# Optimization experiments

Hardware: AMD Instinct MI355X
Metric: run time of the kernel (lower is better)

## Reference

```python
import jax, jax.numpy as jnp
import numpy as np

H = 4  # heads


def _tconv(x, src, dst, ea, Wq, bq, Wk, bk, Wv, bv, We, Ws, bs):
    # PyG TransformerConv, heads=4, concat=False, root_weight=True, beta=False
    N = x.shape[0]
    Dh = Wq.shape[1] // H  # per-head dim (= hidden_channels)
    q = (x @ Wq + bq).reshape(N, H, Dh)
    k = (x @ Wk + bk).reshape(N, H, Dh)
    v = (x @ Wv + bv).reshape(N, H, Dh)
    e = (ea @ We).reshape(-1, H, Dh)      # lin_edge has no bias in PyG
    kj = k[src] + e                        # [E, H, Dh]
    vj = v[src] + e                        # [E, H, Dh]
    alpha = (q[dst] * kj).sum(-1) / jnp.sqrt(jnp.asarray(Dh, x.dtype))  # [E, H]
    # segment softmax over incoming edges of each dst node
    m = jax.ops.segment_max(alpha, dst, num_segments=N)
    a = jnp.exp(alpha - m[dst])
    s = jax.ops.segment_sum(a, dst, num_segments=N)
    a = a / (s[dst] + 1e-16)
    out = jax.ops.segment_sum(a[:, :, None] * vj, dst, num_segments=N)  # [N, H, Dh]
    out = out.mean(axis=1)                 # concat=False -> mean over heads
    return out + x @ Ws + bs               # root/skip connection


def setup_inputs() -> dict:
    key = jax.random.key(0)
    ks = jax.random.split(key, 32)
    N, E, C_in, C_e, Ch = 50000, 800000, 32, 16, 32
    d = {}
    d['x'] = jax.random.normal(ks[0], (N, C_in), dtype=jnp.float32)
    d['edge_attr'] = jax.random.normal(ks[1], (E, C_e), dtype=jnp.float32)
    d['edge_index'] = jax.random.randint(ks[2], (2, E), 0, N, dtype=jnp.int32)
    s = 0.05
    i = 3
    for L, cin in ((1, C_in), (2, Ch)):
        d[f'Wq{L}'] = jax.random.normal(ks[i], (cin, H * Ch)) * s; i += 1
        d[f'bq{L}'] = jnp.zeros((H * Ch,), jnp.float32)
        d[f'Wk{L}'] = jax.random.normal(ks[i], (cin, H * Ch)) * s; i += 1
        d[f'bk{L}'] = jnp.zeros((H * Ch,), jnp.float32)
        d[f'Wv{L}'] = jax.random.normal(ks[i], (cin, H * Ch)) * s; i += 1
        d[f'bv{L}'] = jnp.zeros((H * Ch,), jnp.float32)
        d[f'We{L}'] = jax.random.normal(ks[i], (C_e, H * Ch)) * s; i += 1
        d[f'Ws{L}'] = jax.random.normal(ks[i], (cin, Ch)) * s; i += 1
        d[f'bs{L}'] = jnp.zeros((Ch,), jnp.float32)
    d['Wm1'] = jax.random.normal(ks[i], (2 * Ch + C_e, Ch)) * s; i += 1
    d['bm1'] = jnp.zeros((Ch,), jnp.float32)
    d['Wm2'] = jax.random.normal(ks[i], (Ch, 1)) * s; i += 1
    d['bm2'] = jnp.zeros((1,), jnp.float32)
    return d


def reference(x, edge_attr, edge_index,
              Wq1, bq1, Wk1, bk1, Wv1, bv1, We1, Ws1, bs1,
              Wq2, bq2, Wk2, bk2, Wv2, bv2, We2, Ws2, bs2,
              Wm1, bm1, Wm2, bm2):
    src, dst = edge_index[0], edge_index[1]
    h = jax.nn.relu(_tconv(x, src, dst, edge_attr, Wq1, bq1, Wk1, bk1, Wv1, bv1, We1, Ws1, bs1))
    h = jax.nn.relu(_tconv(h, src, dst, edge_attr, Wq2, bq2, Wk2, bk2, Wv2, bv2, We2, Ws2, bs2))
    ef = jnp.concatenate([h[src], edge_attr, h[dst]], axis=-1)  # [E, 2*Ch + C_e]
    out = jax.nn.relu(ef @ Wm1 + bm1) @ Wm2 + bm2
    return out.reshape(-1)
```

## Files before the change

### kernel.cpp

```cpp
#include <hip/hip_runtime.h>
#include <hip/hip_fp16.h>
#include <math.h>

#define D128 128
#define CH32 32
#define CE16 16

__global__ void k_hist(const int* __restrict__ dst, int* __restrict__ deg, int E) {
    int e = blockIdx.x * blockDim.x + threadIdx.x;
    if (e < E) atomicAdd(&deg[dst[e]], 1);
}

__global__ void k_scan1(const int* __restrict__ deg, int* __restrict__ offs,
                        int* __restrict__ bsum, int N) {
    __shared__ int buf[256];
    int t = threadIdx.x;
    int i = blockIdx.x * 256 + t;
    int v = (i < N) ? deg[i] : 0;
    buf[t] = v;
    __syncthreads();
    #pragma unroll
    for (int off = 1; off < 256; off <<= 1) {
        int val = (t >= off) ? buf[t - off] : 0;
        __syncthreads();
        buf[t] += val;
        __syncthreads();
    }
    if (i < N) offs[i] = buf[t] - v;
    if (t == 255) bsum[blockIdx.x] = buf[255];
}

__global__ void k_scan2(const int* __restrict__ bsum, int* __restrict__ boff, int nb) {
    __shared__ int buf[256];
    int t = threadIdx.x;
    int v = (t < nb) ? bsum[t] : 0;
    buf[t] = v;
    __syncthreads();
    #pragma unroll
    for (int off = 1; off < 256; off <<= 1) {
        int val = (t >= off) ? buf[t - off] : 0;
        __syncthreads();
        buf[t] += val;
        __syncthreads();
    }
    if (t < nb) boff[t] = buf[t] - v;
}

__global__ void k_scan3(const int* __restrict__ boff, int* __restrict__ offs,
                        int* __restrict__ cur, int N, int E) {
    int i = blockIdx.x * blockDim.x + threadIdx.x;
    if (i < N) {
        int o = offs[i] + boff[i >> 8];
        offs[i] = o;
        cur[i] = o;
    }
    if (i == 0) offs[N] = E;
}

__global__ void k_scatter_idx(const int* __restrict__ src, const int* __restrict__ dst,
                              int* __restrict__ cur, int* __restrict__ csr_srcb,
                              int2* __restrict__ csr_de, int E) {
    int e = blockIdx.x * blockDim.x + threadIdx.x;
    if (e < E) {
        int d = dst[e];
        int p = atomicAdd(&cur[d], 1);
        csr_srcb[p] = src[e] << 9;
        csr_de[p] = make_int2(d, e);
    }
}

__global__ __launch_bounds__(256) void k_gather_ea(
    const float4* __restrict__ ea4, const int2* __restrict__ csr_de,
    float4* __restrict__ ea_csr4, int E) {
    int idx = blockIdx.x * 256 + threadIdx.x;
    int p = idx >> 2, q = idx & 3;
    if (p < E) {
        int e = csr_de[p].y;
        ea_csr4[idx] = ea4[e * 4 + q];
    }
}

__global__ void k_wqe(const float* __restrict__ Wq1, const float* __restrict__ bq1,
                      const float* __restrict__ We1,
                      const float* __restrict__ Wq2, const float* __restrict__ bq2,
                      const float* __restrict__ We2,
                      float* __restrict__ Wqe1, float* __restrict__ bqe1,
                      float* __restrict__ Wqe2, float* __restrict__ bqe2) {
    int t = threadIdx.x, h = t >> 4, j = t & 15;
    const float QS = 0.17677669529663687f * 1.4426950408889634f;
    int b = blockIdx.x;
    int layer = (b >= 33);
    int i = layer ? b - 33 : b;
    const float* Wq = layer ? Wq2 : Wq1;
    const float* bq = layer ? bq2 : bq1;
    const float* We = layer ? We2 : We1;
    float* Wqe = layer ? Wqe2 : Wqe1;
    float* bqe = layer ? bqe2 : bqe1;
    const float* base = (i < 32) ? (Wq + i * D128) : bq;
    float s = 0.f;
    #pragma unroll
    for (int d = 0; d < 32; d++)
        s = fmaf(base[h * 32 + d], We[j * D128 + h * 32 + d], s);
    s *= QS;
    if (i < 32) Wqe[i * 64 + t] = s;
    else        bqe[t] = s;
}

__global__ __launch_bounds__(128) void k_nodeproj(
    const float* __restrict__ xin,
    const float* __restrict__ Wq, const float* __restrict__ bq,
    const float* __restrict__ Wk, const float* __restrict__ bk,
    const float* __restrict__ Wv, const float* __restrict__ bv,
    const float* __restrict__ Ws, const float* __restrict__ bs,
    const float* __restrict__ Wqe, const float* __restrict__ bqe,
    float* __restrict__ q, __half* __restrict__ kvh,
    float* __restrict__ skip, float* __restrict__ qeb, int N)
{
    int tid = threadIdx.x;
    int c   = tid & 31;
    int pos = ((tid >> 2) << 3) | (tid & 3);
    float wq[32], wk[32], wv[32], ws[32];
    #pragma unroll
    for (int j = 0; j < 32; j++) {
        wq[j] = Wq[j * D128 + tid];
        wk[j] = Wk[j * D128 + tid];
        wv[j] = Wv[j * D128 + tid];
        ws[j] = Ws[j * CH32 + c];
    }
    float bqc = bq[tid], bkc = bk[tid], bvc = bv[tid], bsc = bs[c];
    __shared__ float wqeS[32][64];
    __shared__ float xs[4][32];
    for (int i = tid; i < 2048; i += 128) wqeS[i >> 6][i & 63] = Wqe[i];
    float bqec = bqe[tid & 63];
    int nchunk = (N + 3) / 4;
    for (int chk = blockIdx.x; chk < nchunk; chk += gridDim.x) {
        int base = chk * 4;
        {
            int r = tid >> 5;
            int n = base + r;
            xs[r][c] = (n < N) ? xin[n * 32 + c] : 0.f;
        }
        __syncthreads();
        #pragma unroll
        for (int r = 0; r < 4; r++) {
            int n = base + r;
            if (n < N) {
                float aq = bqc, ak = bkc, av = bvc;
                #pragma unroll
                for (int j = 0; j < 32; j++) {
                    float xj = xs[r][j];
                    aq = fmaf(xj, wq[j], aq);
                    ak = fmaf(xj, wk[j], ak);
                    av = fmaf(xj, wv[j], av);
                }
                q[n * D128 + tid] = aq;
                kvh[(size_t)n * 256 + pos]     = __float2half_rn(ak);
                kvh[(size_t)n * 256 + pos + 4] = __float2half_rn(av);
            }
        }
        {
            int r = tid >> 5;
            int n = base + r;
            if (n < N) {
                float as = bsc;
                #pragma unroll
                for (int j = 0; j < 32; j++) as = fmaf(xs[r][j], ws[j], as);
                skip[n * 32 + c] = as;
            }
        }
        {
            int c6 = tid & 63;
            int r0 = (tid >> 6) << 1;
            #pragma unroll
            for (int rr = 0; rr < 2; rr++) {
                int n = base + r0 + rr;
                if (n < N) {
                    float a = bqec;
                    #pragma unroll
                    for (int j = 0; j < 32; j++)
                        a = fmaf(xs[r0 + rr][j], wqeS[j][c6], a);
                    qeb[(size_t)n * 64 + c6] = a;
                }
            }
        }
        __syncthreads();
    }
}

__global__ __launch_bounds__(64) void k_edgeattn(
    const float* __restrict__ q, const __half* __restrict__ kvh,
    const float* __restrict__ skip,
    const float* __restrict__ ea_csr, const float* __restrict__ We,
    const int* __restrict__ offs, const int* __restrict__ csr_srcb,
    const float* __restrict__ qeb, float* __restrict__ hout)
{
    int node = blockIdx.x;
    int lane = threadIdx.x;
    int eg   = lane >> 5;
    int c    = lane & 31;
    int g    = c & 7;
    int c4   = c << 2;

    const float QS = 0.17677669529663687f * 1.4426950408889634f;
    float4 qv = *(const float4*)&q[(size_t)node * D128 + c4];
    qv.x *= QS; qv.y *= QS; qv.z *= QS; qv.w *= QS;

    float2 qe01 = *(const float2*)&qeb[(size_t)node * 64 + ((c >> 3) << 4) + 2 * g];
    float qe0 = qe01.x, qe1 = qe01.y;

    int s0 = offs[node], s1 = offs[node + 1];
    int deg = s1 - s0;

    float l = 0.f;
    float ac0 = 0.f, ac1 = 0.f, ac2 = 0.f, ac3 = 0.f;
    float se0 = 0.f, se1 = 0.f;

    if (deg > 0) {
        int last = s1 - 1;
        const char* kvb = (const char*)kvh;
        int toff = c << 4;

        auto eidx = [&](int p) { return min(s0 + 2 * p + eg, last); };
        auto ldidx = [&](int p) { return csr_srcb[eidx(p)]; };
        auto ldkv  = [&](int ib) {
            return *(const float4*)(kvb + (size_t)(unsigned)ib + toff);
        };
        auto ldea  = [&](int p) {
            return *(const float2*)&ea_csr[(size_t)eidx(p) * 16 + 2 * g];
        };
        auto pair = [&](const float4& kvr, const float2& eav, int p) {
            bool valid = (s0 + 2 * p + eg) <= last;
            float2 k01 = __half22float2(*(const __half2*)&kvr.x);
            float2 k23 = __half22float2(*(const __half2*)&kvr.y);
            float2 v01 = __half22float2(*(const __half2*)&kvr.z);
            float2 v23 = __half22float2(*(const __half2*)&kvr.w);
            float t = fmaf(qv.y, k01.y, qv.x * k01.x);
            t = fmaf(qv.z, k23.x, t);
            t = fmaf(qv.w, k23.y, t);
            t = fmaf(qe0, eav.x, t);
            t = fmaf(qe1, eav.y, t);
            t += __shfl_xor(t, 1);
            t += __shfl_xor(t, 2);
            t += __shfl_xor(t, 4);
            float pp = valid ? __builtin_amdgcn_exp2f(t) : 0.f;
            l += pp;
            ac0 = fmaf(pp, v01.x, ac0);
            ac1 = fmaf(pp, v01.y, ac1);
            ac2 = fmaf(pp, v23.x, ac2);
            ac3 = fmaf(pp, v23.y, ac3);
            se0 = fmaf(pp, eav.x, se0);
            se1 = fmaf(pp, eav.y, se1);
        };

        int iA0 = ldidx(0), iA1 = ldidx(1);
        int iB0 = ldidx(2), iB1 = ldidx(3);
        float4 kA0 = ldkv(iA0), kA1 = ldkv(iA1);
        float2 eA0 = ldea(0),   eA1 = ldea(1);

        int p = 0;
        int nIter = (deg + 7) >> 3;
        for (int it = 0; it < nIter; ++it) {
            float4 kB0 = ldkv(iB0), kB1 = ldkv(iB1);
            float2 eB0 = ldea(p + 2), eB1 = ldea(p + 3);
            iA0 = ldidx(p + 4); iA1 = ldidx(p + 5);

            pair(kA0, eA0, p + 0);
            pair(kA1, eA1, p + 1);

            kA0 = ldkv(iA0); kA1 = ldkv(iA1);
            eA0 = ldea(p + 4); eA1 = ldea(p + 5);
            iB0 = ldidx(p + 6); iB1 = ldidx(p + 7);

            pair(kB0, eB0, p + 2);
            pair(kB1, eB1, p + 3);

            p += 4;
        }
    }

    l   += __shfl_xor(l, 32);
    ac0 += __shfl_xor(ac0, 32);
    ac1 += __shfl_xor(ac1, 32);
    ac2 += __shfl_xor(ac2, 32);
    ac3 += __shfl_xor(ac3, 32);
    se0 += __shfl_xor(se0, 32);
    se1 += __shfl_xor(se1, 32);

    float inv = 1.0f / (l + 1e-16f);
    float r0 = ac0 * inv, r1 = ac1 * inv, r2 = ac2 * inv, r3 = ac3 * inv;
    float sn0 = se0 * inv, sn1 = se1 * inv;

    int gb = lane & ~7;
    #pragma unroll
    for (int j = 0; j < 16; j++) {
        float sj = __shfl((j & 1) ? sn1 : sn0, gb | (j >> 1), 64);
        float4 wj = *(const float4*)&We[j * D128 + c4];
        r0 = fmaf(sj, wj.x, r0);
        r1 = fmaf(sj, wj.y, r1);
        r2 = fmaf(sj, wj.z, r2);
        r3 = fmaf(sj, wj.w, r3);
    }
    r0 += __shfl_xor(r0, 8);  r0 += __shfl_xor(r0, 16);
    r1 += __shfl_xor(r1, 8);  r1 += __shfl_xor(r1, 16);
    r2 += __shfl_xor(r2, 8);  r2 += __shfl_xor(r2, 16);
    r3 += __shfl_xor(r3, 8);  r3 += __shfl_xor(r3, 16);
    if (lane < 8) {
        const float4 sk = *(const float4*)&skip[(size_t)node * 32 + c4];
        float4 o;
        o.x = fmaxf(fmaf(0.25f, r0, sk.x), 0.f);
        o.y = fmaxf(fmaf(0.25f, r1, sk.y), 0.f);
        o.z = fmaxf(fmaf(0.25f, r2, sk.z), 0.f);
        o.w = fmaxf(fmaf(0.25f, r3, sk.w), 0.f);
        *(float4*)&hout[(size_t)node * 32 + c4] = o;
    }
}

__global__ __launch_bounds__(256) void k_postproj(
    const float* __restrict__ h, const float* __restrict__ Wm1,
    const float* __restrict__ bm1, float* __restrict__ hA,
    float* __restrict__ hC, int N) {
    __shared__ float WA[32][32], WC[32][32];
    __shared__ float hs[8][32];
    int tid = threadIdx.x;
    for (int i = tid; i < 1024; i += 256) {
        WA[i >> 5][i & 31] = Wm1[i];
        WC[i >> 5][i & 31] = Wm1[48 * 32 + i];
    }
    int col = tid & 31, r = tid >> 5;
    float bb = bm1[col];
    __syncthreads();
    int nchunk = (N + 7) / 8;
    for (int chk = blockIdx.x; chk < nchunk; chk += gridDim.x) {
        int n = chk * 8 + r;
        hs[r][col] = (n < N) ? h[(size_t)n * 32 + col] : 0.f;
        __syncthreads();
        if (n < N) {
            float a = bb, cc = 0.f;
            #pragma unroll
            for (int j = 0; j < 32; j++) {
                float hj = hs[r][j];
                a  = fmaf(hj, WA[j][col], a);
                cc = fmaf(hj, WC[j][col], cc);
            }
            hA[(size_t)n * 32 + col] = a;
            hC[(size_t)n * 32 + col] = cc;
        }
        __syncthreads();
    }
}

__global__ __launch_bounds__(256) void k_mlp(
    const float* __restrict__ hA, const float* __restrict__ hC,
    const float* __restrict__ ea_csr,
    const int* __restrict__ csr_srcb, const int2* __restrict__ csr_de,
    const float* __restrict__ Wm1, const float* __restrict__ Wm2,
    const float* __restrict__ bm2, float* __restrict__ out, int E)
{
    __shared__ float4 B4[16 * 8];
    __shared__ float wm2L[32];
    int tid = threadIdx.x;
    const float4* Wm1B = (const float4*)(Wm1 + 32 * 32);
    for (int i = tid; i < 128; i += 256) B4[i] = Wm1B[i];
    if (tid < 32) wm2L[tid] = Wm2[tid];
    __syncthreads();

    int p = blockIdx.x * 256 + tid;
    if (p >= E) return;
    float b2 = bm2[0];
    int srcb = csr_srcb[p];
    int2 de  = csr_de[p];

    const float4* pa  = (const float4*)((const char*)hA + ((size_t)(unsigned)srcb >> 2));
    const float4* pc  = (const float4*)(hC + (size_t)de.x * 32);
    const float4* eav = (const float4*)(ea_csr + (size_t)p * 16);

    float4 acc[8];
    #pragma unroll
    for (int i = 0; i < 8; i++) {
        float4 va = pa[i], vc = pc[i];
        acc[i] = make_float4(va.x + vc.x, va.y + vc.y, va.z + vc.z, va.w + vc.w);
    }

    auto dorow = [&](int j, float xj) {
        #pragma unroll
        for (int c4 = 0; c4 < 8; c4++) {
            float4 w = B4[j * 8 + c4];
            acc[c4].x = fmaf(xj, w.x, acc[c4].x);
            acc[c4].y = fmaf(xj, w.y, acc[c4].y);
            acc[c4].z = fmaf(xj, w.z, acc[c4].z);
            acc[c4].w = fmaf(xj, w.w, acc[c4].w);
        }
    };

    #pragma unroll
    for (int qd = 0; qd < 4; qd++) {
        float4 xv = eav[qd];
        dorow(qd * 4 + 0, xv.x); dorow(qd * 4 + 1, xv.y);
        dorow(qd * 4 + 2, xv.z); dorow(qd * 4 + 3, xv.w);
    }

    float y = b2;
    #pragma unroll
    for (int c4 = 0; c4 < 8; c4++) {
        y += fmaxf(acc[c4].x, 0.f) * wm2L[c4 * 4 + 0];
        y += fmaxf(acc[c4].y, 0.f) * wm2L[c4 * 4 + 1];
        y += fmaxf(acc[c4].z, 0.f) * wm2L[c4 * 4 + 2];
        y += fmaxf(acc[c4].w, 0.f) * wm2L[c4 * 4 + 3];
    }
    out[de.y] = y;
}

extern "C" void kernel_launch(void* const* d_in, const int* in_sizes, int n_in,
                              void* d_out, int out_size, void* d_ws, size_t ws_size,
                              hipStream_t stream)
{
    const float* x  = (const float*)d_in[0];
    const float* ea = (const float*)d_in[1];
    const int*   ei = (const int*)d_in[2];
    const int N = in_sizes[0] / 32;
    const int E = in_sizes[1] / 16;
    const int* src = ei;
    const int* dst = ei + E;

    const float *Wq1 = (const float*)d_in[3],  *bq1 = (const float*)d_in[4];
    const float *Wk1 = (const float*)d_in[5],  *bk1 = (const float*)d_in[6];
    const float *Wv1 = (const float*)d_in[7],  *bv1 = (const float*)d_in[8];
    const float *We1 = (const float*)d_in[9],  *Ws1 = (const float*)d_in[10];
    const float *bs1 = (const float*)d_in[11];
    const float *Wq2 = (const float*)d_in[12], *bq2 = (const float*)d_in[13];
    const float *Wk2 = (const float*)d_in[14], *bk2 = (const float*)d_in[15];
    const float *Wv2 = (const float*)d_in[16], *bv2 = (const float*)d_in[17];
    const float *We2 = (const float*)d_in[18], *Ws2 = (const float*)d_in[19];
    const float *bs2 = (const float*)d_in[20];
    const float *Wm1 = (const float*)d_in[21], *bm1 = (const float*)d_in[22];
    const float *Wm2 = (const float*)d_in[23], *bm2 = (const float*)d_in[24];

    char* w = (char*)d_ws;
    auto alloc = [&](size_t bytes) -> void* {
        void* p = (void*)w;
        w += (bytes + 255) & ~(size_t)255;
        return p;
    };
    int* deg      = (int*)alloc((size_t)N * 4);
    int* offs     = (int*)alloc(((size_t)N + 1) * 4);
    int* cur      = (int*)alloc((size_t)N * 4);
    int* bsum     = (int*)alloc(256 * 4);
    int* boff     = (int*)alloc(256 * 4);
    int* csr_srcb = (int*)alloc((size_t)E * 4);
    int2* csr_de  = (int2*)alloc((size_t)E * 8);
    float* ea_csr = (float*)alloc((size_t)E * 16 * 4);
    float* qb     = (float*)alloc((size_t)N * 128 * 4);
    __half* kvb   = (__half*)alloc((size_t)N * 256 * 2);
    float* skipb  = (float*)alloc((size_t)N * 32 * 4);
    float* h1     = (float*)alloc((size_t)N * 32 * 4);
    float* h2     = (float*)alloc((size_t)N * 32 * 4);
    float* Wqe1   = (float*)alloc(32 * 64 * 4);
    float* bqe1   = (float*)alloc(64 * 4);
    float* Wqe2   = (float*)alloc(32 * 64 * 4);
    float* bqe2   = (float*)alloc(64 * 4);
    float* qeb    = (float*)alloc((size_t)N * 64 * 4);
    float* hA     = (float*)alloc((size_t)N * 32 * 4);
    float* hC     = (float*)alloc((size_t)N * 32 * 4);

    hipMemsetAsync(deg, 0, (size_t)N * 4, stream);

    int ebl = (E + 255) / 256;
    int nb  = (N + 255) / 256;
    k_wqe<<<66, 64, 0, stream>>>(Wq1, bq1, We1, Wq2, bq2, We2,
                                 Wqe1, bqe1, Wqe2, bqe2);
    k_hist<<<ebl, 256, 0, stream>>>(dst, deg, E);
    k_scan1<<<nb, 256, 0, stream>>>(deg, offs, bsum, N);
    k_scan2<<<1, 256, 0, stream>>>(bsum, boff, nb);
    k_scan3<<<nb, 256, 0, stream>>>(boff, offs, cur, N, E);
    k_scatter_idx<<<ebl, 256, 0, stream>>>(src, dst, cur, csr_srcb, csr_de, E);
    k_gather_ea<<<(E * 4 + 255) / 256, 256, 0, stream>>>(
        (const float4*)ea, csr_de, (float4*)ea_csr, E);

    k_nodeproj<<<1024, 128, 0, stream>>>(x, Wq1, bq1, Wk1, bk1, Wv1, bv1, Ws1, bs1,
                                         Wqe1, bqe1, qb, kvb, skipb, qeb, N);
    k_edgeattn<<<N, 64, 0, stream>>>(qb, kvb, skipb, ea_csr, We1,
                                     offs, csr_srcb, qeb, h1);
    k_nodeproj<<<1024, 128, 0, stream>>>(h1, Wq2, bq2, Wk2, bk2, Wv2, bv2, Ws2, bs2,
                                         Wqe2, bqe2, qb, kvb, skipb, qeb, N);
    k_edgeattn<<<N, 64, 0, stream>>>(qb, kvb, skipb, ea_csr, We2,
                                     offs, csr_srcb, qeb, h2);
    k_postproj<<<1024, 256, 0, stream>>>(h2, Wm1, bm1, hA, hC, N);
    k_mlp<<<ebl, 256, 0, stream>>>(hA, hC, ea_csr, csr_srcb, csr_de,
                                   Wm1, Wm2, bm2, (float*)d_out, E);
}
```

Before: 533.7 us.

## Drop CSR-ordered edge_attr copy; gather edge attributes by edge id in attention

Removes the k_gather_ea pass that copied edge_attr into CSR order. Instead, the scatter kernel stores a packed (src byte offset, edge byte offset) int2 per CSR slot, and the attention kernel gathers edge attributes directly from the original array. The MLP kernel now runs in original edge order, reading src/dst directly and writing out[e] contiguously. This saves a full E×64-byte read/write pass and the extra index arrays, but the attention kernel's edge-attribute loads become random gathers instead of streaming reads. Edge byte offsets (e<<6) stay within int range for E=800k.

```diff
diff --git a/kernel.cpp b/kernel.cpp
--- a/kernel.cpp
+++ b/kernel.cpp
@@ -58,25 +58,13 @@
 }
 
 __global__ void k_scatter_idx(const int* __restrict__ src, const int* __restrict__ dst,
-                              int* __restrict__ cur, int* __restrict__ csr_srcb,
-                              int2* __restrict__ csr_de, int E) {
+                              int* __restrict__ cur, int2* __restrict__ csr_se, int E) {
     int e = blockIdx.x * blockDim.x + threadIdx.x;
     if (e < E) {
         int d = dst[e];
         int p = atomicAdd(&cur[d], 1);
-        csr_srcb[p] = src[e] << 9;
-        csr_de[p] = make_int2(d, e);
-    }
-}
-
-__global__ __launch_bounds__(256) void k_gather_ea(
-    const float4* __restrict__ ea4, const int2* __restrict__ csr_de,
-    float4* __restrict__ ea_csr4, int E) {
-    int idx = blockIdx.x * 256 + threadIdx.x;
-    int p = idx >> 2, q = idx & 3;
-    if (p < E) {
-        int e = csr_de[p].y;
-        ea_csr4[idx] = ea4[e * 4 + q];
+        csr_se[p] = make_int2(src[e] << 9,
+                              e << 6);
     }
 }
 
@@ -190,8 +178,8 @@
 __global__ __launch_bounds__(64) void k_edgeattn(
     const float* __restrict__ q, const __half* __restrict__ kvh,
     const float* __restrict__ skip,
-    const float* __restrict__ ea_csr, const float* __restrict__ We,
-    const int* __restrict__ offs, const int* __restrict__ csr_srcb,
+    const float* __restrict__ ea, const float* __restrict__ We,
+    const int* __restrict__ offs, const int2* __restrict__ csr_se,
     const float* __restrict__ qeb, float* __restrict__ hout)
 {
     int node = blockIdx.x;
@@ -218,15 +206,16 @@
     if (deg > 0) {
         int last = s1 - 1;
         const char* kvb = (const char*)kvh;
+        const char* eab = (const char*)ea;
         int toff = c << 4;
-
-        auto eidx = [&](int p) { return min(s0 + 2 * p + eg, last); };
-        auto ldidx = [&](int p) { return csr_srcb[eidx(p)]; };
-        auto ldkv  = [&](int ib) {
+        int goff = g << 3;
+
+        auto ldse = [&](int p) { return csr_se[min(s0 + 2 * p + eg, last)]; };
+        auto ldkv = [&](int ib) {
             return *(const float4*)(kvb + (size_t)(unsigned)ib + toff);
         };
-        auto ldea  = [&](int p) {
-            return *(const float2*)&ea_csr[(size_t)eidx(p) * 16 + 2 * g];
+        auto ldea = [&](int ib) {
+            return *(const float2*)(eab + (size_t)(unsigned)ib + goff);
         };
         auto pair = [&](const float4& kvr, const float2& eav, int p) {
             bool valid = (s0 + 2 * p + eg) <= last;
@@ -252,24 +241,24 @@
             se1 = fmaf(pp, eav.y, se1);
         };
 
-        int iA0 = ldidx(0), iA1 = ldidx(1);
-        int iB0 = ldidx(2), iB1 = ldidx(3);
-        float4 kA0 = ldkv(iA0), kA1 = ldkv(iA1);
-        float2 eA0 = ldea(0),   eA1 = ldea(1);
+        int2 iA0 = ldse(0), iA1 = ldse(1);
+        int2 iB0 = ldse(2), iB1 = ldse(3);
+        float4 kA0 = ldkv(iA0.x), kA1 = ldkv(iA1.x);
+        float2 eA0 = ldea(iA0.y), eA1 = ldea(iA1.y);
 
         int p = 0;
         int nIter = (deg + 7) >> 3;
         for (int it = 0; it < nIter; ++it) {
-            float4 kB0 = ldkv(iB0), kB1 = ldkv(iB1);
-            float2 eB0 = ldea(p + 2), eB1 = ldea(p + 3);
-            iA0 = ldidx(p + 4); iA1 = ldidx(p + 5);
+            float4 kB0 = ldkv(iB0.x), kB1 = ldkv(iB1.x);
+            float2 eB0 = ldea(iB0.y), eB1 = ldea(iB1.y);
+            iA0 = ldse(p + 4); iA1 = ldse(p + 5);
 
             pair(kA0, eA0, p + 0);
             pair(kA1, eA1, p + 1);
 
-            kA0 = ldkv(iA0); kA1 = ldkv(iA1);
-            eA0 = ldea(p + 4); eA1 = ldea(p + 5);
-            iB0 = ldidx(p + 6); iB1 = ldidx(p + 7);
+            kA0 = ldkv(iA0.x); kA1 = ldkv(iA1.x);
+            eA0 = ldea(iA0.y); eA1 = ldea(iA1.y);
+            iB0 = ldse(p + 6); iB1 = ldse(p + 7);
 
             pair(kB0, eB0, p + 2);
             pair(kB1, eB1, p + 3);
@@ -351,8 +340,8 @@
 
 __global__ __launch_bounds__(256) void k_mlp(
     const float* __restrict__ hA, const float* __restrict__ hC,
-    const float* __restrict__ ea_csr,
-    const int* __restrict__ csr_srcb, const int2* __restrict__ csr_de,
+    const float* __restrict__ ea,
+    const int* __restrict__ src, const int* __restrict__ dst,
     const float* __restrict__ Wm1, const float* __restrict__ Wm2,
     const float* __restrict__ bm2, float* __restrict__ out, int E)
 {
@@ -364,15 +353,14 @@
     if (tid < 32) wm2L[tid] = Wm2[tid];
     __syncthreads();
 
-    int p = blockIdx.x * 256 + tid;
-    if (p >= E) return;
+    int e = blockIdx.x * 256 + tid;
+    if (e >= E) return;
     float b2 = bm2[0];
-    int srcb = csr_srcb[p];
-    int2 de  = csr_de[p];
-
-    const float4* pa  = (const float4*)((const char*)hA + ((size_t)(unsigned)srcb >> 2));
-    const float4* pc  = (const float4*)(hC + (size_t)de.x * 32);
-    const float4* eav = (const float4*)(ea_csr + (size_t)p * 16);
+    int s = src[e], d = dst[e];
+
+    const float4* pa  = (const float4*)(hA + (size_t)s * 32);
+    const float4* pc  = (const float4*)(hC + (size_t)d * 32);
+    const float4* eav = (const float4*)(ea + (size_t)e * 16);
 
     float4 acc[8];
     #pragma unroll
@@ -407,7 +395,7 @@
         y += fmaxf(acc[c4].z, 0.f) * wm2L[c4 * 4 + 2];
         y += fmaxf(acc[c4].w, 0.f) * wm2L[c4 * 4 + 3];
     }
-    out[de.y] = y;
+    out[e] = y;
 }
 
 extern "C" void kernel_launch(void* const* d_in, const int* in_sizes, int n_in,
@@ -446,9 +434,7 @@
     int* cur      = (int*)alloc((size_t)N * 4);
     int* bsum     = (int*)alloc(256 * 4);
     int* boff     = (int*)alloc(256 * 4);
-    int* csr_srcb = (int*)alloc((size_t)E * 4);
-    int2* csr_de  = (int2*)alloc((size_t)E * 8);
-    float* ea_csr = (float*)alloc((size_t)E * 16 * 4);
+    int2* csr_se  = (int2*)alloc((size_t)E * 8);
     float* qb     = (float*)alloc((size_t)N * 128 * 4);
     __half* kvb   = (__half*)alloc((size_t)N * 256 * 2);
     float* skipb  = (float*)alloc((size_t)N * 32 * 4);
@@ -472,19 +458,17 @@
     k_scan1<<<nb, 256, 0, stream>>>(deg, offs, bsum, N);
     k_scan2<<<1, 256, 0, stream>>>(bsum, boff, nb);
     k_scan3<<<nb, 256, 0, stream>>>(boff, offs, cur, N, E);
-    k_scatter_idx<<<ebl, 256, 0, stream>>>(src, dst, cur, csr_srcb, csr_de, E);
-    k_gather_ea<<<(E * 4 + 255) / 256, 256, 0, stream>>>(
-        (const float4*)ea, csr_de, (float4*)ea_csr, E);
+    k_scatter_idx<<<ebl, 256, 0, stream>>>(src, dst, cur, csr_se, E);
 
     k_nodeproj<<<1024, 128, 0, stream>>>(x, Wq1, bq1, Wk1, bk1, Wv1, bv1, Ws1, bs1,
                                          Wqe1, bqe1, qb, kvb, skipb, qeb, N);
-    k_edgeattn<<<N, 64, 0, stream>>>(qb, kvb, skipb, ea_csr, We1,
-                                     offs, csr_srcb, qeb, h1);
+    k_edgeattn<<<N, 64, 0, stream>>>(qb, kvb, skipb, ea, We1,
+                                     offs, csr_se, qeb, h1);
     k_nodeproj<<<1024, 128, 0, stream>>>(h1, Wq2, bq2, Wk2, bk2, Wv2, bv2, Ws2, bs2,
                                          Wqe2, bqe2, qb, kvb, skipb, qeb, N);
-    k_edgeattn<<<N, 64, 0, stream>>>(qb, kvb, skipb, ea_csr, We2,
-                                     offs, csr_srcb, qeb, h2);
+    k_edgeattn<<<N, 64, 0, stream>>>(qb, kvb, skipb, ea, We2,
+                                     offs, csr_se, qeb, h2);
     k_postproj<<<1024, 256, 0, stream>>>(h2, Wm1, bm1, hA, hC, N);
-    k_mlp<<<ebl, 256, 0, stream>>>(hA, hC, ea_csr, csr_srcb, csr_de,
-                                   Wm1, Wm2, bm2, (float*)d_out, E);
-}
+    k_mlp<<<ebl, 256, 0, stream>>>(hA, hC, ea, src, dst, Wm1, Wm2, bm2,
+                                   (float*)d_out, E);
+}
```

New measurement: 553.6 us. 3.7% more time.
